# Optimization experiments

Hardware: AMD Instinct MI355X
Metric: run time of the kernel (lower is better)

The kernel has to match this reference:

```python
import math
import jax, jax.numpy as jnp
import numpy as np

B, T, D = 2, 2048, 2048
H = 16
HD = D // H  # 128


def setup_inputs() -> dict:
    key = jax.random.key(0)
    k1, k2, k3 = jax.random.split(key, 3)
    x = jax.random.normal(k1, (B, T, D), dtype=jnp.float32)
    # Linear weights stored as [in, out] for x @ W (torch Linear weight is [out,in])
    w_attn = jax.random.normal(k2, (D, 3 * D), dtype=jnp.float32) * (1.0 / math.sqrt(D))
    w_proj = jax.random.normal(k3, (D, D), dtype=jnp.float32) * (1.0 / math.sqrt(D))
    return {"x": x, "w_attn": w_attn, "w_proj": w_proj}


def reference(x, w_attn, w_proj):
    Bc, Tc, Dc = x.shape
    qkv = x @ w_attn  # [B, T, 3D]
    q, k, v = jnp.split(qkv, 3, axis=2)
    # [B, H, T, HD]
    q = q.reshape(Bc, Tc, H, HD).transpose(0, 2, 1, 3)
    k = k.reshape(Bc, Tc, H, HD).transpose(0, 2, 1, 3)
    v = v.reshape(Bc, Tc, H, HD).transpose(0, 2, 1, 3)
    att = jnp.einsum('bhqd,bhkd->bhqk', q, k) * (1.0 / math.sqrt(HD))
    causal = jnp.tril(jnp.ones((Tc, Tc), dtype=bool))
    att = jnp.where(causal[None, None], att, -jnp.inf)
    att = jax.nn.softmax(att, axis=-1)
    y = jnp.einsum('bhqk,bhkd->bhqd', att, v)
    y = y.transpose(0, 2, 1, 3).reshape(Bc, Tc, Dc)
    return y @ w_proj
```

## Files before the change

kernel.cpp:

```cpp
#include <hip/hip_runtime.h>
#include <hip/hip_bf16.h>

#define B_ 2
#define T_ 2048
#define D_ 2048
#define H_ 16
#define HD_ 128
#define N3_ (3 * D_)
#define M_ (B_ * T_)

typedef __attribute__((ext_vector_type(8))) short short8;
typedef __attribute__((ext_vector_type(4))) short short4v;
typedef __attribute__((ext_vector_type(4))) float floatx4;

__device__ __forceinline__ ushort f2bf(float f) {
  unsigned int x = __float_as_uint(f);
  unsigned int r = (x + 0x7fffu + ((x >> 16) & 1u)) >> 16;
  return (ushort)r;
}

__device__ __forceinline__ void gload_lds16(const ushort* g, ushort* l) {
  __builtin_amdgcn_global_load_lds(
      (const __attribute__((address_space(1))) void*)g,
      (__attribute__((address_space(3))) void*)l, 16, 0, 0);
}

#define CONVB 4096
#define WATB 12288
#define WPTB 4096
__global__ __launch_bounds__(256) void prep(const float* __restrict__ x,
                                            const float* __restrict__ wa,
                                            const float* __restrict__ wp,
                                            ushort* __restrict__ xb,
                                            ushort* __restrict__ wt_attn,
                                            ushort* __restrict__ wt_proj) {
  __shared__ ushort tile[32][33];
  int bid = blockIdx.x;
  if (bid < CONVB) {
    int i = bid * 2048 + threadIdx.x * 8;
    union { ushort u[8]; short8 v; } t;
#pragma unroll
    for (int j = 0; j < 8; j++) t.u[j] = f2bf(x[i + j]);
    *(short8*)(xb + i) = t.v;
    return;
  }
  const float* in;
  ushort* out;
  int N, bx, by;
  if (bid < CONVB + WATB) {
    int id = bid - CONVB;
    N = N3_; bx = id % 192; by = id / 192; in = wa; out = wt_attn;
  } else {
    int id = bid - (CONVB + WATB);
    N = D_; bx = id & 63; by = id >> 6; in = wp; out = wt_proj;
  }
  int n0 = bx * 32, k0 = by * 32;
  int tx = threadIdx.x & 31, ty = threadIdx.x >> 5;
#pragma unroll
  for (int i = ty; i < 32; i += 8)
    tile[i][tx] = f2bf(in[(size_t)(k0 + i) * N + n0 + tx]);
  __syncthreads();
#pragma unroll
  for (int i = ty; i < 32; i += 8)
    out[(size_t)(n0 + i) * 2048 + k0 + tx] = tile[tx][i];
}

#define GBM 256
#define GBN 128
#define GBK 32
#define GKD 2048
#define GNT (GKD / GBK)
#define A_US (GBM * GBK)
#define B_US (GBN * GBK)
#define BUF_US (A_US + B_US)

struct GPtr {
  const ushort* a0;
  const ushort* a1;
  const ushort* b0;
};

template <bool STG, int VM>
__device__ __forceinline__ void ktile(const GPtr& gp, size_t kpos,
                                      const ushort* Ac, const ushort* Bc,
                                      ushort* As_s, ushort* Bs_s, int w512,
                                      const int (&arow)[4], const int (&brow)[4],
                                      floatx4 (&acc)[4][4]) {
  short8 af[4], bf[4];
#pragma unroll
  for (int mi = 0; mi < 4; mi++)
    af[mi] = *(const short8*)(Ac + arow[mi]);
#pragma unroll
  for (int nj = 0; nj < 4; nj++)
    bf[nj] = *(const short8*)(Bc + brow[nj]);
  if constexpr (STG) {
    gload_lds16(gp.a0 + kpos, As_s + w512);
    gload_lds16(gp.a1 + kpos, As_s + 4096 + w512);
    gload_lds16(gp.b0 + kpos, Bs_s + w512);
  }
  __builtin_amdgcn_s_barrier();
  asm volatile("s_waitcnt lgkmcnt(0)" ::: "memory");
  __builtin_amdgcn_sched_barrier(0);
  __builtin_amdgcn_s_setprio(1);
#pragma unroll
  for (int mi = 0; mi < 4; mi++)
#pragma unroll
    for (int nj = 0; nj < 4; nj++)
      acc[mi][nj] = __builtin_amdgcn_mfma_f32_16x16x32_bf16(
          af[mi], bf[nj], acc[mi][nj], 0, 0, 0);
  __builtin_amdgcn_s_setprio(0);
  if constexpr (VM == 6) {
    asm volatile("s_waitcnt vmcnt(6)" ::: "memory");
    __builtin_amdgcn_sched_barrier(0);
  } else if constexpr (VM == 3) {
    asm volatile("s_waitcnt vmcnt(3)" ::: "memory");
    __builtin_amdgcn_sched_barrier(0);
  } else if constexpr (VM == 0) {
    asm volatile("s_waitcnt vmcnt(0)" ::: "memory");
    __builtin_amdgcn_sched_barrier(0);
  }
  __builtin_amdgcn_s_barrier();
}

__device__ __forceinline__ void gemm_core(const ushort* __restrict__ Ag,
                                          const ushort* __restrict__ Bg,
                                          ushort* lds, floatx4 (&acc)[4][4]) {
  int tid = threadIdx.x;
  int lane = tid & 63, wave = tid >> 6;
  int l16 = lane & 15, quad = lane >> 4;
  int wr = wave >> 1, wc = wave & 1;
  int w512 = wave * 512;

  int swz = ((tid & 3) ^ ((tid >> 3) & 3)) * 8;
  GPtr gp;
  gp.a0 = Ag + (size_t)(tid >> 2) * GKD + swz;
  gp.a1 = gp.a0 + (size_t)128 * GKD;
  gp.b0 = Bg + (size_t)(tid >> 2) * GKD + swz;

  int rchk = (quad ^ ((l16 >> 1) & 3)) * 8;
  int arow[4], brow[4];
#pragma unroll
  for (int i = 0; i < 4; i++) {
    arow[i] = (wr * 64 + i * 16 + l16) * GBK + rchk;
    brow[i] = (wc * 64 + i * 16 + l16) * GBK + rchk;
  }

#pragma unroll
  for (int t = 0; t < 3; t++) {
    ushort* As_s = lds + t * BUF_US;
    gload_lds16(gp.a0 + (size_t)t * GBK, As_s + w512);
    gload_lds16(gp.a1 + (size_t)t * GBK, As_s + 4096 + w512);
    gload_lds16(gp.b0 + (size_t)t * GBK, As_s + A_US + w512);
  }
  asm volatile("s_waitcnt vmcnt(6)" ::: "memory");
  __builtin_amdgcn_sched_barrier(0);
  __builtin_amdgcn_s_barrier();

  int ci = 0, si = 3;
#pragma unroll 1
  for (int t = 0; t < GNT - 3; ++t) {
    const ushort* bc = lds + ci * BUF_US;
    ushort* bs = lds + si * BUF_US;
    ktile<true, 6>(gp, (size_t)(t + 3) * GBK, bc, bc + A_US, bs, bs + A_US,
                   w512, arow, brow, acc);
    ci = (ci + 1) & 3;
    si = (si + 1) & 3;
  }
  const ushort* bc = lds + ci * BUF_US;
  ci = (ci + 1) & 3;
  ktile<false, 3>(gp, 0, bc, bc + A_US, lds, lds + A_US, w512, arow, brow, acc);
  bc = lds + ci * BUF_US;
  ci = (ci + 1) & 3;
  ktile<false, 0>(gp, 0, bc, bc + A_US, lds, lds + A_US, w512, arow, brow, acc);
  bc = lds + ci * BUF_US;
  ktile<false, -1>(gp, 0, bc, bc + A_US, lds, lds + A_US, w512, arow, brow,
                   acc);
}

__global__ __launch_bounds__(512, 2) void gemm_qkv(const ushort* __restrict__ X,
                                                   const ushort* __restrict__ Wt,
                                                   ushort* __restrict__ qb,
                                                   ushort* __restrict__ kb,
                                                   ushort* __restrict__ vst) {
  __shared__ __align__(16) ushort lds[4 * BUF_US];
  floatx4 acc[4][4];
#pragma unroll
  for (int i = 0; i < 4; i++)
#pragma unroll
    for (int j = 0; j < 4; j++) acc[i][j] = (floatx4){0.f, 0.f, 0.f, 0.f};

  int m0 = blockIdx.y * GBM, n0 = blockIdx.x * GBN;
  gemm_core(X + (size_t)m0 * GKD, Wt + (size_t)n0 * GKD, lds, acc);

  int tid = threadIdx.x, lane = tid & 63, wave = tid >> 6;
  int l16 = lane & 15, quad = lane >> 4, wr = wave >> 1, wc = wave & 1;
  int region = n0 >> 11;
  int h = (n0 & 2047) >> 7;
  int b = m0 >> 11, tb = m0 & 2047;
  if (region == 0) {
    ushort* P = qb + ((size_t)(b * H_ + h) * T_ + tb) * HD_;
#pragma unroll
    for (int mi = 0; mi < 4; mi++)
#pragma unroll
      for (int nj = 0; nj < 4; nj++)
#pragma unroll
        for (int r = 0; r < 4; r++)
          P[(size_t)(wr * 64 + mi * 16 + quad * 4 + r) * HD_ + wc * 64 +
            nj * 16 + l16] = f2bf(acc[mi][nj][r]);
  } else if (region == 1) {
    ushort* base = kb + (size_t)(b * H_ + h) * T_ * HD_;
#pragma unroll
    for (int mi = 0; mi < 4; mi++)
#pragma unroll
      for (int nj = 0; nj < 4; nj++) {
        int d = wc * 64 + nj * 16 + l16;
        int dhi = d >> 5, dlo = d & 31;
#pragma unroll
        for (int r = 0; r < 4; r++) {
          int t = tb + wr * 64 + mi * 16 + quad * 4 + r;
          int sK = ((quad * 4 + r) >> 1) & 3;
          base[(size_t)(t >> 6) * 8192 + dhi * 2048 + (t & 63) * 32 +
               (dlo ^ (sK << 3))] = f2bf(acc[mi][nj][r]);
        }
      }
  } else {
    ushort* base = vst + (size_t)(b * H_ + h) * T_ * HD_;
    int sd = ((l16 >> 1) & 3) << 3;
#pragma unroll
    for (int mi = 0; mi < 4; mi++)
#pragma unroll
      for (int r = 0; r < 4; r++) {
        int t = tb + wr * 64 + mi * 16 + quad * 4 + r;
        int c = t & 63;
        int p = (c & 15) * 4 + (c >> 4);
        size_t rowbase =
            (size_t)(t >> 6) * 8192 + (p >> 5) * 4096 + ((p & 31) ^ sd);
#pragma unroll
        for (int nj = 0; nj < 4; nj++) {
          int d = wc * 64 + nj * 16 + l16;
          base[rowbase + d * 32] = f2bf(acc[mi][nj][r]);
        }
      }
  }
}

__global__ __launch_bounds__(512, 2) void gemm_proj(const ushort* __restrict__ Y,
                                                    const ushort* __restrict__ Wt,
                                                    float* __restrict__ out) {
  __shared__ __align__(16) ushort lds[4 * BUF_US];
  floatx4 acc[4][4];
#pragma unroll
  for (int i = 0; i < 4; i++)
#pragma unroll
    for (int j = 0; j < 4; j++) acc[i][j] = (floatx4){0.f, 0.f, 0.f, 0.f};

  int m0 = blockIdx.y * GBM, n0 = blockIdx.x * GBN;
  gemm_core(Y + (size_t)m0 * GKD, Wt + (size_t)n0 * GKD, lds, acc);

  int tid = threadIdx.x, lane = tid & 63, wave = tid >> 6;
  int l16 = lane & 15, quad = lane >> 4, wr = wave >> 1, wc = wave & 1;
#pragma unroll
  for (int mi = 0; mi < 4; mi++)
#pragma unroll
    for (int nj = 0; nj < 4; nj++)
#pragma unroll
      for (int r = 0; r < 4; r++)
        out[(size_t)(m0 + wr * 64 + mi * 16 + quad * 4 + r) * D_ + n0 +
            wc * 64 + nj * 16 + l16] = acc[mi][nj][r];
}

__global__ __launch_bounds__(256) void attn128(const ushort* __restrict__ qb,
                                               const ushort* __restrict__ kst,
                                               const ushort* __restrict__ vst,
                                               ushort* __restrict__ y) {
  __shared__ ushort Ks[8192];
  __shared__ ushort Vs[8192];
  __shared__ ushort Ps[8192];
  int bid = blockIdx.x;
  int bh = bid & 31;
  int qt = (bid < 256) ? (bid >> 5) : (15 - ((bid - 256) >> 5));
  int q0 = qt * 128;
  int tid = threadIdx.x, lane = tid & 63, wave = tid >> 6;
  int l16 = lane & 15, quad = lane >> 4;
  int b = bh >> 4, h = bh & 15;
  const ushort* Q = qb + (size_t)bh * T_ * HD_;
  const ushort* Kt = kst + (size_t)bh * T_ * HD_;
  const ushort* Vt = vst + (size_t)bh * T_ * HD_;
  int qw0 = q0 + wave * 32;

  short8 qf[2][4];
#pragma unroll
  for (int mi = 0; mi < 2; mi++)
#pragma unroll
    for (int kk = 0; kk < 4; kk++)
      qf[mi][kk] = *(const short8*)(Q + (size_t)(qw0 + mi * 16 + l16) * HD_ +
                                    kk * 32 + quad * 8);

  floatx4 o[2][8];
#pragma unroll
  for (int mi = 0; mi < 2; mi++)
#pragma unroll
    for (int nt = 0; nt < 8; nt++) o[mi][nt] = (floatx4){0.f, 0.f, 0.f, 0.f};
  float lrow[2][4];
#pragma unroll
  for (int mi = 0; mi < 2; mi++)
#pragma unroll
    for (int r = 0; r < 4; r++) lrow[mi][r] = 0.f;

  const float scale2 = 0.08838834764831845f * 1.4426950408889634f;
  int ktiles = (q0 >> 6) + 2;
  int vchk = (quad ^ ((l16 >> 1) & 3)) * 8;

  for (int tile = 0; tile < ktiles; tile++) {
    int kt = tile << 6;
    __syncthreads();
#pragma unroll
    for (int i = 0; i < 4; i++) {
      int g = i * 256 + wave * 64;
      gload_lds16(Kt + (size_t)tile * 8192 + (g + lane) * 8, Ks + g * 8);
      gload_lds16(Vt + (size_t)tile * 8192 + (g + lane) * 8, Vs + g * 8);
    }
    __syncthreads();
    if (kt <= qw0 + 31) {
      floatx4 s[2][4];
#pragma unroll
      for (int mi = 0; mi < 2; mi++)
#pragma unroll
        for (int ng = 0; ng < 4; ng++) s[mi][ng] = (floatx4){0.f, 0.f, 0.f, 0.f};
#pragma unroll
      for (int kk = 0; kk < 4; kk++) {
        short8 kf[4];
#pragma unroll
        for (int ng = 0; ng < 4; ng++)
          kf[ng] = *(const short8*)(Ks + kk * 2048 + (ng * 16 + l16) * 32 +
                                    vchk);
#pragma unroll
        for (int mi = 0; mi < 2; mi++)
#pragma unroll
          for (int ng = 0; ng < 4; ng++)
            s[mi][ng] = __builtin_amdgcn_mfma_f32_16x16x32_bf16(
                qf[mi][kk], kf[ng], s[mi][ng], 0, 0, 0);
      }
      if (kt + 63 > qw0) {
#pragma unroll
        for (int mi = 0; mi < 2; mi++)
#pragma unroll
          for (int ng = 0; ng < 4; ng++)
#pragma unroll
            for (int r = 0; r < 4; r++) {
              int key = kt + ng * 16 + l16;
              int qr = qw0 + mi * 16 + quad * 4 + r;
              float p =
                  (key <= qr) ? exp2f(s[mi][ng][r] * scale2) : 0.f;
              s[mi][ng][r] = p;
              lrow[mi][r] += p;
            }
      } else {
#pragma unroll
        for (int mi = 0; mi < 2; mi++)
#pragma unroll
          for (int ng = 0; ng < 4; ng++)
#pragma unroll
            for (int r = 0; r < 4; r++) {
              float p = exp2f(s[mi][ng][r] * scale2);
              s[mi][ng][r] = p;
              lrow[mi][r] += p;
            }
      }
      ushort* Pw = Ps + wave * 2048;
#pragma unroll
      for (int mi = 0; mi < 2; mi++)
#pragma unroll
        for (int r = 0; r < 4; r++) {
          int row = mi * 16 + quad * 4 + r;
          short4v pk;
#pragma unroll
          for (int ng = 0; ng < 4; ng++) pk[ng] = (short)f2bf(s[mi][ng][r]);
          *(short4v*)(Pw + row * 64 + (((l16 >> 1) ^ (row & 7)) << 3) +
                      ((l16 & 1) << 2)) = pk;
        }
      short8 pf[2][2];
#pragma unroll
      for (int mi = 0; mi < 2; mi++)
#pragma unroll
        for (int kc = 0; kc < 2; kc++) {
          int row = mi * 16 + l16;
          pf[mi][kc] = *(const short8*)(
              Pw + row * 64 + ((((kc << 2) + quad) ^ (row & 7)) << 3));
        }
#pragma unroll
      for (int kc = 0; kc < 2; kc++)
#pragma unroll
        for (int nt = 0; nt < 8; nt++) {
          short8 vf = *(const short8*)(Vs + kc * 4096 + (nt * 16 + l16) * 32 +
                                       vchk);
#pragma unroll
          for (int mi = 0; mi < 2; mi++)
            o[mi][nt] = __builtin_amdgcn_mfma_f32_16x16x32_bf16(
                pf[mi][kc], vf, o[mi][nt], 0, 0, 0);
        }
    }
  }

#pragma unroll
  for (int off = 1; off < 16; off <<= 1)
#pragma unroll
    for (int mi = 0; mi < 2; mi++)
#pragma unroll
      for (int r = 0; r < 4; r++)
        lrow[mi][r] += __shfl_xor(lrow[mi][r], off);

#pragma unroll
  for (int mi = 0; mi < 2; mi++)
#pragma unroll
    for (int r = 0; r < 4; r++) {
      float inv = 1.f / lrow[mi][r];
      int t = qw0 + mi * 16 + quad * 4 + r;
#pragma unroll
      for (int nt = 0; nt < 8; nt++)
        y[((size_t)(b * T_ + t)) * D_ + h * HD_ + nt * 16 + l16] =
            f2bf(o[mi][nt][r] * inv);
    }
}

extern "C" void kernel_launch(void* const* d_in, const int* in_sizes, int n_in,
                              void* d_out, int out_size, void* d_ws,
                              size_t ws_size, hipStream_t stream) {
  const float* x = (const float*)d_in[0];
  const float* w_attn = (const float*)d_in[1];
  const float* w_proj = (const float*)d_in[2];
  float* out = (float*)d_out;

  char* ws = (char*)d_ws;
  ushort* wt_attn = (ushort*)(ws);
  ushort* wt_proj = (ushort*)(ws + 25165824);
  ushort* qb = (ushort*)(ws + 33554432);
  ushort* kb = (ushort*)(ws + 50331648);
  ushort* vst = (ushort*)(ws + 67108864);
  ushort* xb = (ushort*)(ws + 83886080);
  ushort* yb = xb;
  (void)in_sizes; (void)n_in; (void)out_size; (void)ws_size;

  prep<<<CONVB + WATB + WPTB, 256, 0, stream>>>(x, w_attn, w_proj, xb,
                                                wt_attn, wt_proj);
  gemm_qkv<<<dim3(N3_ / GBN, M_ / GBM), 512, 0, stream>>>(xb, wt_attn, qb, kb,
                                                          vst);
  attn128<<<B_ * H_ * (T_ / 128), 256, 0, stream>>>(qb, kb, vst, yb);
  gemm_proj<<<dim3(D_ / GBN, M_ / GBM), 512, 0, stream>>>(yb, wt_proj, out);
}
```

Before: 380.0 us.

## Deepen GEMM K-tile to 64 with 3-stage ring; double-buffer attention K/V

```diff
diff --git a/kernel.cpp b/kernel.cpp
--- a/kernel.cpp
+++ b/kernel.cpp
@@ -67,7 +67,7 @@
 
 #define GBM 256
 #define GBN 128
-#define GBK 32
+#define GBK 64
 #define GKD 2048
 #define GNT (GKD / GBK)
 #define A_US (GBM * GBK)
@@ -76,50 +76,56 @@
 
 struct GPtr {
   const ushort* a0;
-  const ushort* a1;
   const ushort* b0;
 };
 
-template <bool STG, int VM>
-__device__ __forceinline__ void ktile(const GPtr& gp, size_t kpos,
+__device__ __forceinline__ void gstage(const GPtr& gp, size_t kpos,
+                                       ushort* slot, int w512) {
+#pragma unroll
+  for (int j = 0; j < 4; j++)
+    gload_lds16(gp.a0 + kpos + (size_t)j * 64 * GKD, slot + j * 4096 + w512);
+#pragma unroll
+  for (int j = 0; j < 2; j++)
+    gload_lds16(gp.b0 + kpos + (size_t)j * 64 * GKD,
+                slot + A_US + j * 4096 + w512);
+}
+
+template <int VM, bool STG, bool BAR>
+__device__ __forceinline__ void kstep(const GPtr& gp, size_t kpos,
                                       const ushort* Ac, const ushort* Bc,
-                                      ushort* As_s, ushort* Bs_s, int w512,
-                                      const int (&arow)[4], const int (&brow)[4],
+                                      ushort* sslot, int w512,
+                                      const int (&aoff)[4][2],
+                                      const int (&boff)[4][2],
                                       floatx4 (&acc)[4][4]) {
-  short8 af[4], bf[4];
-#pragma unroll
-  for (int mi = 0; mi < 4; mi++)
-    af[mi] = *(const short8*)(Ac + arow[mi]);
-#pragma unroll
-  for (int nj = 0; nj < 4; nj++)
-    bf[nj] = *(const short8*)(Bc + brow[nj]);
-  if constexpr (STG) {
-    gload_lds16(gp.a0 + kpos, As_s + w512);
-    gload_lds16(gp.a1 + kpos, As_s + 4096 + w512);
-    gload_lds16(gp.b0 + kpos, Bs_s + w512);
-  }
-  __builtin_amdgcn_s_barrier();
-  asm volatile("s_waitcnt lgkmcnt(0)" ::: "memory");
-  __builtin_amdgcn_sched_barrier(0);
+  short8 af[4][2], bf[4][2];
+#pragma unroll
+  for (int kk = 0; kk < 2; kk++)
+#pragma unroll
+    for (int i = 0; i < 4; i++) {
+      af[i][kk] = *(const short8*)(Ac + aoff[i][kk]);
+      bf[i][kk] = *(const short8*)(Bc + boff[i][kk]);
+    }
+  if constexpr (STG) gstage(gp, kpos, sslot, w512);
   __builtin_amdgcn_s_setprio(1);
 #pragma unroll
-  for (int mi = 0; mi < 4; mi++)
-#pragma unroll
-    for (int nj = 0; nj < 4; nj++)
-      acc[mi][nj] = __builtin_amdgcn_mfma_f32_16x16x32_bf16(
-          af[mi], bf[nj], acc[mi][nj], 0, 0, 0);
+  for (int kk = 0; kk < 2; kk++)
+#pragma unroll
+    for (int mi = 0; mi < 4; mi++)
+#pragma unroll
+      for (int nj = 0; nj < 4; nj++)
+        acc[mi][nj] = __builtin_amdgcn_mfma_f32_16x16x32_bf16(
+            af[mi][kk], bf[nj][kk], acc[mi][nj], 0, 0, 0);
   __builtin_amdgcn_s_setprio(0);
   if constexpr (VM == 6) {
     asm volatile("s_waitcnt vmcnt(6)" ::: "memory");
-    __builtin_amdgcn_sched_barrier(0);
-  } else if constexpr (VM == 3) {
-    asm volatile("s_waitcnt vmcnt(3)" ::: "memory");
-    __builtin_amdgcn_sched_barrier(0);
   } else if constexpr (VM == 0) {
     asm volatile("s_waitcnt vmcnt(0)" ::: "memory");
+  }
+  if constexpr (BAR) {
     __builtin_amdgcn_sched_barrier(0);
-  }
-  __builtin_amdgcn_s_barrier();
+    __builtin_amdgcn_s_barrier();
+    __builtin_amdgcn_sched_barrier(0);
+  }
 }
 
 __device__ __forceinline__ void gemm_core(const ushort* __restrict__ Ag,
@@ -131,50 +137,40 @@
   int wr = wave >> 1, wc = wave & 1;
   int w512 = wave * 512;
 
-  int swz = ((tid & 3) ^ ((tid >> 3) & 3)) * 8;
+  int swz = ((tid & 7) ^ ((tid >> 3) & 7)) * 8;
   GPtr gp;
-  gp.a0 = Ag + (size_t)(tid >> 2) * GKD + swz;
-  gp.a1 = gp.a0 + (size_t)128 * GKD;
-  gp.b0 = Bg + (size_t)(tid >> 2) * GKD + swz;
-
-  int rchk = (quad ^ ((l16 >> 1) & 3)) * 8;
-  int arow[4], brow[4];
-#pragma unroll
-  for (int i = 0; i < 4; i++) {
-    arow[i] = (wr * 64 + i * 16 + l16) * GBK + rchk;
-    brow[i] = (wc * 64 + i * 16 + l16) * GBK + rchk;
-  }
-
-#pragma unroll
-  for (int t = 0; t < 3; t++) {
-    ushort* As_s = lds + t * BUF_US;
-    gload_lds16(gp.a0 + (size_t)t * GBK, As_s + w512);
-    gload_lds16(gp.a1 + (size_t)t * GBK, As_s + 4096 + w512);
-    gload_lds16(gp.b0 + (size_t)t * GBK, As_s + A_US + w512);
-  }
+  gp.a0 = Ag + (size_t)(tid >> 3) * GKD + swz;
+  gp.b0 = Bg + (size_t)(tid >> 3) * GKD + swz;
+
+  int aoff[4][2], boff[4][2];
+#pragma unroll
+  for (int i = 0; i < 4; i++)
+#pragma unroll
+    for (int kk = 0; kk < 2; kk++) {
+      int chk = ((kk * 4 + quad) ^ (l16 & 7)) * 8;
+      aoff[i][kk] = (wr * 64 + i * 16 + l16) * GBK + chk;
+      boff[i][kk] = (wc * 64 + i * 16 + l16) * GBK + chk;
+    }
+
+  gstage(gp, 0, lds, w512);
+  gstage(gp, GBK, lds + BUF_US, w512);
   asm volatile("s_waitcnt vmcnt(6)" ::: "memory");
   __builtin_amdgcn_sched_barrier(0);
   __builtin_amdgcn_s_barrier();
-
-  int ci = 0, si = 3;
+  __builtin_amdgcn_sched_barrier(0);
+
+  const ushort* cp = lds;
+  ushort* sp = lds + 2 * BUF_US;
 #pragma unroll 1
-  for (int t = 0; t < GNT - 3; ++t) {
-    const ushort* bc = lds + ci * BUF_US;
-    ushort* bs = lds + si * BUF_US;
-    ktile<true, 6>(gp, (size_t)(t + 3) * GBK, bc, bc + A_US, bs, bs + A_US,
-                   w512, arow, brow, acc);
-    ci = (ci + 1) & 3;
-    si = (si + 1) & 3;
-  }
-  const ushort* bc = lds + ci * BUF_US;
-  ci = (ci + 1) & 3;
-  ktile<false, 3>(gp, 0, bc, bc + A_US, lds, lds + A_US, w512, arow, brow, acc);
-  bc = lds + ci * BUF_US;
-  ci = (ci + 1) & 3;
-  ktile<false, 0>(gp, 0, bc, bc + A_US, lds, lds + A_US, w512, arow, brow, acc);
-  bc = lds + ci * BUF_US;
-  ktile<false, -1>(gp, 0, bc, bc + A_US, lds, lds + A_US, w512, arow, brow,
-                   acc);
+  for (int t = 0; t < GNT - 2; ++t) {
+    kstep<6, true, true>(gp, (size_t)(t + 2) * GBK, cp, cp + A_US, sp, w512,
+                         aoff, boff, acc);
+    cp = (cp == lds + 2 * BUF_US) ? lds : cp + BUF_US;
+    sp = (sp == lds + 2 * BUF_US) ? lds : sp + BUF_US;
+  }
+  kstep<0, false, true>(gp, 0, cp, cp + A_US, lds, w512, aoff, boff, acc);
+  cp = (cp == lds + 2 * BUF_US) ? lds : cp + BUF_US;
+  kstep<-1, false, false>(gp, 0, cp, cp + A_US, lds, w512, aoff, boff, acc);
 }
 
 __global__ __launch_bounds__(512, 2) void gemm_qkv(const ushort* __restrict__ X,
@@ -182,7 +178,7 @@
                                                    ushort* __restrict__ qb,
                                                    ushort* __restrict__ kb,
                                                    ushort* __restrict__ vst) {
-  __shared__ __align__(16) ushort lds[4 * BUF_US];
+  __shared__ __align__(16) ushort lds[3 * BUF_US];
   floatx4 acc[4][4];
 #pragma unroll
   for (int i = 0; i < 4; i++)
@@ -247,7 +243,7 @@
 __global__ __launch_bounds__(512, 2) void gemm_proj(const ushort* __restrict__ Y,
                                                     const ushort* __restrict__ Wt,
                                                     float* __restrict__ out) {
-  __shared__ __align__(16) ushort lds[4 * BUF_US];
+  __shared__ __align__(16) ushort lds[3 * BUF_US];
   floatx4 acc[4][4];
 #pragma unroll
   for (int i = 0; i < 4; i++)
@@ -273,8 +269,8 @@
                                                const ushort* __restrict__ kst,
                                                const ushort* __restrict__ vst,
                                                ushort* __restrict__ y) {
-  __shared__ ushort Ks[8192];
-  __shared__ ushort Vs[8192];
+  __shared__ ushort Ks[2][8192];
+  __shared__ ushort Vs[2][8192];
   __shared__ ushort Ps[8192];
   int bid = blockIdx.x;
   int bh = bid & 31;
@@ -311,17 +307,30 @@
   int ktiles = (q0 >> 6) + 2;
   int vchk = (quad ^ ((l16 >> 1) & 3)) * 8;
 
+#pragma unroll
+  for (int i = 0; i < 4; i++) {
+    int g = i * 256 + wave * 64;
+    gload_lds16(Kt + (g + lane) * 8, Ks[0] + g * 8);
+    gload_lds16(Vt + (g + lane) * 8, Vs[0] + g * 8);
+  }
+  __syncthreads();
+
+  int cur = 0;
   for (int tile = 0; tile < ktiles; tile++) {
     int kt = tile << 6;
-    __syncthreads();
-#pragma unroll
-    for (int i = 0; i < 4; i++) {
-      int g = i * 256 + wave * 64;
-      gload_lds16(Kt + (size_t)tile * 8192 + (g + lane) * 8, Ks + g * 8);
-      gload_lds16(Vt + (size_t)tile * 8192 + (g + lane) * 8, Vs + g * 8);
+    if (tile + 1 < ktiles) {
+#pragma unroll
+      for (int i = 0; i < 4; i++) {
+        int g = i * 256 + wave * 64;
+        gload_lds16(Kt + (size_t)(tile + 1) * 8192 + (g + lane) * 8,
+                    Ks[cur ^ 1] + g * 8);
+        gload_lds16(Vt + (size_t)(tile + 1) * 8192 + (g + lane) * 8,
+                    Vs[cur ^ 1] + g * 8);
+      }
     }
-    __syncthreads();
     if (kt <= qw0 + 31) {
+      const ushort* Ksb = Ks[cur];
+      const ushort* Vsb = Vs[cur];
       floatx4 s[2][4];
 #pragma unroll
       for (int mi = 0; mi < 2; mi++)
@@ -332,14 +341,16 @@
         short8 kf[4];
 #pragma unroll
         for (int ng = 0; ng < 4; ng++)
-          kf[ng] = *(const short8*)(Ks + kk * 2048 + (ng * 16 + l16) * 32 +
+          kf[ng] = *(const short8*)(Ksb + kk * 2048 + (ng * 16 + l16) * 32 +
                                     vchk);
+        __builtin_amdgcn_s_setprio(1);
 #pragma unroll
         for (int mi = 0; mi < 2; mi++)
 #pragma unroll
           for (int ng = 0; ng < 4; ng++)
             s[mi][ng] = __builtin_amdgcn_mfma_f32_16x16x32_bf16(
                 qf[mi][kk], kf[ng], s[mi][ng], 0, 0, 0);
+        __builtin_amdgcn_s_setprio(0);
       }
       if (kt + 63 > qw0) {
 #pragma unroll
@@ -389,17 +400,22 @@
               Pw + row * 64 + ((((kc << 2) + quad) ^ (row & 7)) << 3));
         }
 #pragma unroll
-      for (int kc = 0; kc < 2; kc++)
+      for (int kc = 0; kc < 2; kc++) {
 #pragma unroll
         for (int nt = 0; nt < 8; nt++) {
-          short8 vf = *(const short8*)(Vs + kc * 4096 + (nt * 16 + l16) * 32 +
+          short8 vf = *(const short8*)(Vsb + kc * 4096 + (nt * 16 + l16) * 32 +
                                        vchk);
+          __builtin_amdgcn_s_setprio(1);
 #pragma unroll
           for (int mi = 0; mi < 2; mi++)
             o[mi][nt] = __builtin_amdgcn_mfma_f32_16x16x32_bf16(
                 pf[mi][kc], vf, o[mi][nt], 0, 0, 0);
+          __builtin_amdgcn_s_setprio(0);
         }
+      }
     }
+    __syncthreads();
+    cur ^= 1;
   }
 
 #pragma unroll
```

Measured after the change: 371.1 us. 2.3% less time.
